# Performance work log

Measured on AMD Instinct MI355X. Metric: run time of the kernel, lower is better.

## Reference

```python
import jax, jax.numpy as jnp
import numpy as np

NUM_CLASSES = 172
IGNORE_INDEX = 255
DICE_WEIGHT = 0.5
EPS = 1e-7


def setup_inputs() -> dict:
    key = jax.random.key(0)
    k1, k2 = jax.random.split(key)
    pred = jax.random.normal(k1, (4, NUM_CLASSES, 256, 256), dtype=jnp.float32)
    target = jax.random.randint(k2, (4, 256, 256), 0, NUM_CLASSES, dtype=jnp.int32)
    return {"pred": pred, "target": target}


def reference(pred, target):
    # pred: [B, C, H, W] logits; target: [B, H, W] int labels (255 = ignore)
    C = NUM_CLASSES
    logp = jax.nn.log_softmax(pred, axis=1)  # [B, C, H, W]

    # ---- cross entropy with ignore_index (mean over valid pixels) ----
    valid = target != IGNORE_INDEX  # [B, H, W]
    safe_tgt = jnp.where(valid, target, 0)
    nll = -jnp.take_along_axis(logp, safe_tgt[:, None].astype(jnp.int32), axis=1)[:, 0]  # [B, H, W]
    n_valid = jnp.sum(valid)
    ce = jnp.sum(jnp.where(valid, nll, 0.0)) / jnp.maximum(n_valid, 1).astype(pred.dtype)

    # ---- dice loss: vectorized over classes (replaces per-class python loop) ----
    p = jnp.exp(logp)  # softmax probs [B, C, H, W]
    # intersection[c] = sum over pixels with target==c of p[:, c] at those pixels
    gathered = jnp.take_along_axis(p, safe_tgt[:, None].astype(jnp.int32), axis=1)[:, 0]  # [B, H, W]
    seg_ids = target.ravel().astype(jnp.int32)  # ignore pixels land in bucket 255, discarded
    inter = jax.ops.segment_sum(gathered.ravel(), seg_ids, num_segments=256)[:C]  # [C]
    counts = jax.ops.segment_sum(jnp.ones_like(gathered.ravel()), seg_ids, num_segments=256)[:C]
    union = jnp.sum(p, axis=(0, 2, 3)) + counts  # [C]
    valid_c = union > 0
    dice_terms = jnp.where(valid_c, (2.0 * inter + EPS) / (union + EPS), 0.0)
    n_valid_c = jnp.sum(valid_c).astype(pred.dtype)
    dice = jnp.where(n_valid_c > 0, 1.0 - jnp.sum(dice_terms) / jnp.maximum(n_valid_c, 1.0), 0.0)

    return ce + DICE_WEIGHT * dice
```

## Files before the change

kernel.cpp:

```cpp
#include <hip/hip_runtime.h>
#include <stdint.h>

#define NCLS 172
#define HALF 86
#define IGN 255
#define HW 65536
#define NPIX 262144
#define EPSV 1e-7f
#define NSTAGE 16
#define SSTRIDE 520
#define USTRIDE 65

__device__ __forceinline__ float waveReduceSum(float v) {
    #pragma unroll
    for (int off = 32; off > 0; off >>= 1) v += __shfl_down(v, off, 64);
    return v;
}

__global__ __launch_bounds__(512) void seg_main(
    const float* __restrict__ pred, const int* __restrict__ tgt,
    float* __restrict__ part)
{
    __shared__ float ldsU[NCLS * USTRIDE];
    __shared__ float sEx[512 * 4];
    __shared__ float ldsInter[NCLS];
    __shared__ unsigned int ldsCnt[NCLS];
    __shared__ float ldsRed[16];

    const int tid  = threadIdx.x;
    const int half = tid >> 8;
    const int qid  = tid & 255;
    const int lane = tid & 63;
    const int wave = tid >> 6;

    for (int i = tid; i < NCLS * USTRIDE; i += 512) ldsU[i] = 0.f;
    for (int i = tid; i < NCLS; i += 512) { ldsInter[i] = 0.f; ldsCnt[i] = 0u; }
    if (tid < 16) ldsRed[tid] = 0.f;
    __syncthreads();

    const int pix0 = blockIdx.x * 1024 + qid * 4;
    const int b    = pix0 >> 16;
    const int hw   = pix0 & (HW - 1);
    const float*  bp   = pred + (size_t)b * NCLS * HW + hw;
    const float4* base = (const float4*)bp;
    const int c0 = half * HALF;

    float s0 = 0.f, s1 = 0.f, s2 = 0.f, s3 = 0.f;
    #pragma unroll 8
    for (int i = 0; i < HALF; ++i) {
        float4 x = base[(size_t)(c0 + i) * (HW / 4)];
        s0 += __expf(x.x); s1 += __expf(x.y); s2 += __expf(x.z); s3 += __expf(x.w);
    }
    ((float4*)sEx)[tid] = make_float4(s0, s1, s2, s3);
    __syncthreads();
    const float4 o = ((float4*)sEx)[tid ^ 256];
    const float sf0 = s0 + o.x, sf1 = s1 + o.y, sf2 = s2 + o.z, sf3 = s3 + o.w;
    const float iv0 = 1.f / sf0, iv1 = 1.f / sf1, iv2 = 1.f / sf2, iv3 = 1.f / sf3;

    #pragma unroll 8
    for (int i = 0; i < HALF; ++i) {
        const int c = c0 + i;
        float4 x = base[(size_t)c * (HW / 4)];
        float d = __expf(x.x) * iv0 + __expf(x.y) * iv1
                + __expf(x.z) * iv2 + __expf(x.w) * iv3;
        atomicAdd(&ldsU[c * USTRIDE + lane], d);
    }

    float nllS = 0.f, nvS = 0.f;
    if (half == 0) {
        const int4 t4 = *(const int4*)(tgt + pix0);
        const int   tv[4]  = { t4.x, t4.y, t4.z, t4.w };
        const float sfv[4] = { sf0, sf1, sf2, sf3 };
        const float ivv[4] = { iv0, iv1, iv2, iv3 };
        #pragma unroll
        for (int j = 0; j < 4; ++j) {
            const int t = tv[j];
            if (t != IGN) {
                const float xt = bp[(size_t)t * HW + j];
                nllS += __logf(sfv[j]) - xt;
                nvS  += 1.f;
                atomicAdd(&ldsInter[t], __expf(xt) * ivv[j]);
                atomicAdd(&ldsCnt[t], 1u);
            }
        }
    }
    float vr = waveReduceSum(nllS);
    float nr = waveReduceSum(nvS);
    if (lane == 0) { ldsRed[wave] = vr; ldsRed[8 + wave] = nr; }
    __syncthreads();

    float* pb = part + (size_t)(blockIdx.x & (NSTAGE - 1)) * SSTRIDE;
    for (int c = tid; c < NCLS; c += 512) {
        float u = 0.f;
        #pragma unroll 16
        for (int j = 0; j < 64; ++j) u += ldsU[c * USTRIDE + j];
        atomicAdd(&pb[344 + c], u);
        float vi = ldsInter[c];
        if (vi != 0.f) atomicAdd(&pb[c], vi);
        unsigned int ci = ldsCnt[c];
        if (ci != 0u) atomicAdd(&pb[172 + c], (float)ci);
    }
    if (tid == 0) {
        float cs = 0.f;
        #pragma unroll
        for (int w = 0; w < 8; ++w) cs += ldsRed[w];
        atomicAdd(&pb[516], cs);
    }
    if (tid == 1) {
        float ns = 0.f;
        #pragma unroll
        for (int w = 0; w < 8; ++w) ns += ldsRed[8 + w];
        atomicAdd(&pb[517], ns);
    }
}

__global__ __launch_bounds__(256) void seg_fin(const float* __restrict__ part,
                                               float* __restrict__ out)
{
    __shared__ float sT[256], sN[256];
    const int tid = threadIdx.x;
    float term = 0.f, nv = 0.f;
    if (tid < NCLS) {
        float inter = 0.f, cnt = 0.f, uni = 0.f;
        #pragma unroll
        for (int st = 0; st < NSTAGE; ++st) {
            const float* pb = part + st * SSTRIDE;
            inter += pb[tid];
            cnt   += pb[172 + tid];
            uni   += pb[344 + tid];
        }
        float u = uni + cnt;
        if (u > 0.f) { term = (2.f * inter + EPSV) / (u + EPSV); nv = 1.f; }
    }
    sT[tid] = term; sN[tid] = nv;
    __syncthreads();
    #pragma unroll
    for (int s2 = 128; s2 > 0; s2 >>= 1) {
        if (tid < s2) { sT[tid] += sT[tid + s2]; sN[tid] += sN[tid + s2]; }
        __syncthreads();
    }
    if (tid == 0) {
        float ce = 0.f, nvl = 0.f;
        #pragma unroll
        for (int st = 0; st < NSTAGE; ++st) {
            ce  += part[st * SSTRIDE + 516];
            nvl += part[st * SSTRIDE + 517];
        }
        float ceo  = ce / fmaxf(nvl, 1.f);
        float dice = (sN[0] > 0.f) ? (1.f - sT[0] / fmaxf(sN[0], 1.f)) : 0.f;
        out[0] = ceo + 0.5f * dice;
    }
}

extern "C" void kernel_launch(void* const* d_in, const int* in_sizes, int n_in,
                              void* d_out, int out_size, void* d_ws, size_t ws_size,
                              hipStream_t stream) {
    const float* pred = (const float*)d_in[0];
    const int*   tgt  = (const int*)d_in[1];
    float* out  = (float*)d_out;
    float* part = (float*)d_ws;

    hipMemsetAsync(d_ws, 0, NSTAGE * SSTRIDE * sizeof(float), stream);
    seg_main<<<NPIX / 1024, 512, 0, stream>>>(pred, tgt, part);
    seg_fin<<<1, 256, 0, stream>>>(part, out);
}
```

Before: 308.9 us.

## Retile main kernel to 256-pixel blocks with 4 waves interleaving classes

Each block now handles 256 pixels with 256 threads. The four waves split the 172 classes in interleaved strides of 4, so every wave does fully coalesced float4 loads across its 64 lanes. That gives 4x more blocks, which should improve occupancy and spread of work across CUs. The LDS union buffer is shrunk to 32 slots per class, the reciprocal now uses rcp, and the block reductions are simplified. In exchange there are four times more global atomics into the staged partial buffers and more LDS atomic contention per slot.

```diff
diff --git a/kernel.cpp b/kernel.cpp
--- a/kernel.cpp
+++ b/kernel.cpp
@@ -2,116 +2,106 @@
 #include <stdint.h>
 
 #define NCLS 172
-#define HALF 86
+#define NWAVE 4
+#define CPW 43
 #define IGN 255
 #define HW 65536
 #define NPIX 262144
+#define TILE 256
 #define EPSV 1e-7f
 #define NSTAGE 16
 #define SSTRIDE 520
-#define USTRIDE 65
+#define USTR 33
 
-__device__ __forceinline__ float waveReduceSum(float v) {
-    #pragma unroll
-    for (int off = 32; off > 0; off >>= 1) v += __shfl_down(v, off, 64);
-    return v;
-}
-
-__global__ __launch_bounds__(512) void seg_main(
+__global__ __launch_bounds__(256) void seg_main(
     const float* __restrict__ pred, const int* __restrict__ tgt,
     float* __restrict__ part)
 {
-    __shared__ float ldsU[NCLS * USTRIDE];
-    __shared__ float sEx[512 * 4];
+    __shared__ float ldsU[NCLS * USTR];
+    __shared__ float4 sEx[NWAVE * 64];
     __shared__ float ldsInter[NCLS];
     __shared__ unsigned int ldsCnt[NCLS];
-    __shared__ float ldsRed[16];
+    __shared__ float ldsRed[2];
 
     const int tid  = threadIdx.x;
-    const int half = tid >> 8;
-    const int qid  = tid & 255;
+    const int w    = tid >> 6;
     const int lane = tid & 63;
-    const int wave = tid >> 6;
 
-    for (int i = tid; i < NCLS * USTRIDE; i += 512) ldsU[i] = 0.f;
-    for (int i = tid; i < NCLS; i += 512) { ldsInter[i] = 0.f; ldsCnt[i] = 0u; }
-    if (tid < 16) ldsRed[tid] = 0.f;
+    for (int i = tid; i < NCLS * USTR; i += 256) ldsU[i] = 0.f;
+    for (int i = tid; i < NCLS; i += 256) { ldsInter[i] = 0.f; ldsCnt[i] = 0u; }
     __syncthreads();
 
-    const int pix0 = blockIdx.x * 1024 + qid * 4;
+    const int pix0 = blockIdx.x * TILE;
     const int b    = pix0 >> 16;
-    const int hw   = pix0 & (HW - 1);
-    const float*  bp   = pred + (size_t)b * NCLS * HW + hw;
-    const float4* base = (const float4*)bp;
-    const int c0 = half * HALF;
+    const int hw0  = pix0 & (HW - 1);
+    const float*  bp    = pred + (size_t)b * NCLS * HW + hw0;
+    const float4* base4 = (const float4*)bp;
 
-    float s0 = 0.f, s1 = 0.f, s2 = 0.f, s3 = 0.f;
+    float4 sq = make_float4(0.f, 0.f, 0.f, 0.f);
     #pragma unroll 8
-    for (int i = 0; i < HALF; ++i) {
-        float4 x = base[(size_t)(c0 + i) * (HW / 4)];
-        s0 += __expf(x.x); s1 += __expf(x.y); s2 += __expf(x.z); s3 += __expf(x.w);
+    for (int i = 0; i < CPW; ++i) {
+        float4 x = base4[(size_t)(w + 4 * i) * (HW / 4) + lane];
+        sq.x += __expf(x.x); sq.y += __expf(x.y);
+        sq.z += __expf(x.z); sq.w += __expf(x.w);
     }
-    ((float4*)sEx)[tid] = make_float4(s0, s1, s2, s3);
+    sEx[w * 64 + lane] = sq;
     __syncthreads();
-    const float4 o = ((float4*)sEx)[tid ^ 256];
-    const float sf0 = s0 + o.x, sf1 = s1 + o.y, sf2 = s2 + o.z, sf3 = s3 + o.w;
-    const float iv0 = 1.f / sf0, iv1 = 1.f / sf1, iv2 = 1.f / sf2, iv3 = 1.f / sf3;
+    const float4 a0 = sEx[lane], a1 = sEx[64 + lane], a2 = sEx[128 + lane], a3 = sEx[192 + lane];
+    const float4 sf = make_float4((a0.x + a1.x) + (a2.x + a3.x),
+                                  (a0.y + a1.y) + (a2.y + a3.y),
+                                  (a0.z + a1.z) + (a2.z + a3.z),
+                                  (a0.w + a1.w) + (a2.w + a3.w));
+    const float4 iv = make_float4(__builtin_amdgcn_rcpf(sf.x), __builtin_amdgcn_rcpf(sf.y),
+                                  __builtin_amdgcn_rcpf(sf.z), __builtin_amdgcn_rcpf(sf.w));
 
     #pragma unroll 8
-    for (int i = 0; i < HALF; ++i) {
-        const int c = c0 + i;
-        float4 x = base[(size_t)c * (HW / 4)];
-        float d = __expf(x.x) * iv0 + __expf(x.y) * iv1
-                + __expf(x.z) * iv2 + __expf(x.w) * iv3;
-        atomicAdd(&ldsU[c * USTRIDE + lane], d);
+    for (int i = 0; i < CPW; ++i) {
+        const int c = w + 4 * i;
+        float4 x = base4[(size_t)c * (HW / 4) + lane];
+        float d = __expf(x.x) * iv.x + __expf(x.y) * iv.y
+                + __expf(x.z) * iv.z + __expf(x.w) * iv.w;
+        atomicAdd(&ldsU[c * USTR + (lane & 31)], d);
     }
 
-    float nllS = 0.f, nvS = 0.f;
-    if (half == 0) {
-        const int4 t4 = *(const int4*)(tgt + pix0);
+    if (w == 0) {
+        const int4 t4 = *(const int4*)(tgt + pix0 + 4 * lane);
         const int   tv[4]  = { t4.x, t4.y, t4.z, t4.w };
-        const float sfv[4] = { sf0, sf1, sf2, sf3 };
-        const float ivv[4] = { iv0, iv1, iv2, iv3 };
+        const float sfv[4] = { sf.x, sf.y, sf.z, sf.w };
+        const float ivv[4] = { iv.x, iv.y, iv.z, iv.w };
+        float nllS = 0.f, nvS = 0.f;
         #pragma unroll
         for (int j = 0; j < 4; ++j) {
             const int t = tv[j];
             if (t != IGN) {
-                const float xt = bp[(size_t)t * HW + j];
+                const float xt = bp[(size_t)t * HW + 4 * lane + j];
                 nllS += __logf(sfv[j]) - xt;
                 nvS  += 1.f;
                 atomicAdd(&ldsInter[t], __expf(xt) * ivv[j]);
                 atomicAdd(&ldsCnt[t], 1u);
             }
         }
+        #pragma unroll
+        for (int off = 32; off > 0; off >>= 1) {
+            nllS += __shfl_down(nllS, off, 64);
+            nvS  += __shfl_down(nvS,  off, 64);
+        }
+        if (lane == 0) { ldsRed[0] = nllS; ldsRed[1] = nvS; }
     }
-    float vr = waveReduceSum(nllS);
-    float nr = waveReduceSum(nvS);
-    if (lane == 0) { ldsRed[wave] = vr; ldsRed[8 + wave] = nr; }
     __syncthreads();
 
     float* pb = part + (size_t)(blockIdx.x & (NSTAGE - 1)) * SSTRIDE;
-    for (int c = tid; c < NCLS; c += 512) {
+    for (int c = tid; c < NCLS; c += 256) {
         float u = 0.f;
-        #pragma unroll 16
-        for (int j = 0; j < 64; ++j) u += ldsU[c * USTRIDE + j];
+        #pragma unroll
+        for (int j = 0; j < 32; ++j) u += ldsU[c * USTR + j];
         atomicAdd(&pb[344 + c], u);
         float vi = ldsInter[c];
         if (vi != 0.f) atomicAdd(&pb[c], vi);
         unsigned int ci = ldsCnt[c];
         if (ci != 0u) atomicAdd(&pb[172 + c], (float)ci);
     }
-    if (tid == 0) {
-        float cs = 0.f;
-        #pragma unroll
-        for (int w = 0; w < 8; ++w) cs += ldsRed[w];
-        atomicAdd(&pb[516], cs);
-    }
-    if (tid == 1) {
-        float ns = 0.f;
-        #pragma unroll
-        for (int w = 0; w < 8; ++w) ns += ldsRed[8 + w];
-        atomicAdd(&pb[517], ns);
-    }
+    if (tid == 0) atomicAdd(&pb[516], ldsRed[0]);
+    if (tid == 1) atomicAdd(&pb[517], ldsRed[1]);
 }
 
 __global__ __launch_bounds__(256) void seg_fin(const float* __restrict__ part,
@@ -161,6 +151,6 @@
     float* part = (float*)d_ws;
 
     hipMemsetAsync(d_ws, 0, NSTAGE * SSTRIDE * sizeof(float), stream);
-    seg_main<<<NPIX / 1024, 512, 0, stream>>>(pred, tgt, part);
+    seg_main<<<NPIX / TILE, 256, 0, stream>>>(pred, tgt, part);
     seg_fin<<<1, 256, 0, stream>>>(part, out);
 }
```

Result: no change. 303.6 us (-1.7%).
